# Performance work log

Hardware: AMD Instinct MI355X
Metric: run time of the kernel (lower is better)

The kernel has to match this reference:

```python
import jax, jax.numpy as jnp
import numpy as np

QMIN, QMAX = -128.0, 127.0          # int-8 symmetric range
CONST_N = 15.0                      # shift-exp range constant
OUT_BIT = 8                         # const_output_bit
INT32_MAX = 2.0 ** 31 - 1.0


def setup_inputs() -> dict:
    key = jax.random.key(0)
    kx, ks = jax.random.split(key)
    x = jax.random.normal(kx, (4, 2048, 4096), dtype=jnp.float32)
    # per-channel quantizer scale ~ abs-max / 127 statistics
    scaler = jnp.max(jnp.abs(x), axis=(0, 1)) / 127.0 + 1e-6  # [D]
    return {"x": x, "scaler": scaler}


def _int_exp_shift(x_int, sf):
    # x_int ~ integer-valued float tensor; sf per-channel scaling factor [D]
    x_int = x_int + jnp.floor(x_int / 2.0) - jnp.floor(x_int / 16.0)  # *1.4375 ~ /ln2
    x0 = jnp.floor(-1.0 / sf)                     # [D], negative
    x_int = jnp.maximum(x_int, CONST_N * x0)
    q = jnp.floor(x_int / x0)
    r = x_int - x0 * q
    e = r / 2.0 - x0
    return jnp.maximum(jnp.floor(e * jnp.exp2(CONST_N - q)), 0.0)


def reference(x, scaler):
    # quantize input per-channel (int8 grid, kept in float)
    pre_x_int = jnp.clip(jnp.round(x / scaler), QMIN, QMAX)
    sf_sig = scaler * 1.702

    x_int_max = jnp.max(pre_x_int, axis=-1, keepdims=True)   # [B,S,1]
    x_int = pre_x_int - x_int_max

    exp_int = _int_exp_shift(x_int, sf_sig)                  # [B,S,D]
    exp_int_max = _int_exp_shift(-x_int_max, sf_sig)         # [B,S,D] (bcast)
    exp_sum = jnp.minimum(exp_int + exp_int_max, INT32_MAX)

    factor = jnp.floor(INT32_MAX / exp_sum)
    sigmoid_int = jnp.floor(exp_int * factor / 2.0 ** (31 - OUT_BIT + 1))

    sigmoid_scale = 1.0 / 2.0 ** (OUT_BIT - 1)    # 1/128
    y = pre_x_int * sigmoid_int * (scaler * sigmoid_scale)
    return y
```

## Files before the change

### kernel.cpp

```cpp
#include <hip/hip_runtime.h>


#define D 4096
#define BLK 512
#define CPT 8
#define RPB 8
#define NW (BLK / 64)
#define NSLOT 12
#define TENT (NSLOT * 256)
#define EPS 1e-4f
#define F2_31 2147483648.0f

typedef float f32x4 __attribute__((ext_vector_type(4)));

__device__ __forceinline__ float exp_fast(float xi, float nx0, float rx0) {
    const float q = floorf(fmaf(xi, rx0, EPS));
    const float r = fmaf(nx0, q, xi);
    const float e = fmaf(r, 0.5f, nx0);
    return floorf(ldexpf(e, 15 - (int)q));
}

__device__ __forceinline__ float exp_slow(float xi, float x0) {
    xi = fmaxf(xi, 15.0f * x0);
    const float q = floorf(xi / x0);
    const float r = fmaf(-x0, q, xi);
    const float e = fmaf(r, 0.5f, -x0);
    return fmaxf(floorf(e * ldexpf(1.0f, 15 - (int)q)), 0.0f);
}

__global__ __launch_bounds__(BLK) void quantgelu_kernel(
    const float* __restrict__ x, const float* __restrict__ scaler,
    float* __restrict__ out, int nrows)
{
    const int tid  = threadIdx.x;
    const int wid  = tid >> 6;
    const int lane = tid & 63;
    const int row0 = blockIdx.x * RPB;

    __shared__ __align__(16) float smax2[2][NW];
    __shared__ float eit[TENT];
    __shared__ float siga[TENT];
    __shared__ float sigb[TENT];

    const int c0 = tid * 4;
    const int c1 = BLK * 4 + tid * 4;

    long long base = (long long)row0 * D;
    float4 xv[4];
    if (row0 < nrows) {
        xv[0] = *reinterpret_cast<const float4*>(x + base + c0);
        xv[1] = *reinterpret_cast<const float4*>(x + base + c1);
    }
    if (row0 + 1 < nrows) {
        xv[2] = *reinterpret_cast<const float4*>(x + base + D + c0);
        xv[3] = *reinterpret_cast<const float4*>(x + base + D + c1);
    }

    float s_[CPT], rs_[CPT], x0_[CPT];
    #pragma unroll
    for (int k = 0; k < 2; ++k) {
        const float4 sv = *reinterpret_cast<const float4*>(scaler + (k ? c1 : c0));
        const float ss[4] = {sv.x, sv.y, sv.z, sv.w};
        #pragma unroll
        for (int j = 0; j < 4; ++j) {
            const int i = k * 4 + j;
            const float s = ss[j];
            s_[i]  = s;
            rs_[i] = 1.0f / s;
            x0_[i] = floorf(-1.0f / (s * 1.702f));
        }
    }

    float x0mn = x0_[0], x0mx = x0_[0];
    #pragma unroll
    for (int i = 1; i < CPT; ++i) {
        x0mn = fminf(x0mn, x0_[i]);
        x0mx = fmaxf(x0mx, x0_[i]);
    }
    #pragma unroll
    for (int off = 1; off < 64; off <<= 1) {
        x0mn = fminf(x0mn, __shfl_xor(x0mn, off));
        x0mx = fmaxf(x0mx, __shfl_xor(x0mx, off));
    }
    if (lane == 0) { smax2[0][wid] = x0mn; smax2[1][wid] = x0mx; }
    __syncthreads();
    #pragma unroll
    for (int w = 0; w < NW; ++w) {
        x0mn = fminf(x0mn, smax2[0][w]);
        x0mx = fmaxf(x0mx, smax2[1][w]);
    }
    __syncthreads();

    const int  nslots = (int)(x0mx - x0mn) + 1;
    const bool ok = (x0mn >= -64.0f) && (nslots <= NSLOT);
    const int  nent = nslots << 8;

    int bo_[CPT];
    #pragma unroll
    for (int i = 0; i < CPT; ++i)
        bo_[i] = ((int)(x0_[i] - x0mn)) << 8;

    const float x0l  = x0mn + (float)lane;
    const float nx0l = -x0l;
    const float rx0l = 1.0f / x0l;
    const float c15l = 15.0f * x0l;

    if (ok) {
        for (int e = tid; e < nent; e += BLK) {
            const int   slot = e >> 8;
            const float x0v  = x0mn + (float)slot;
            float xi = -(float)(e & 255);
            xi = xi + floorf(xi * 0.5f) - floorf(xi * 0.0625f);
            xi = fmaxf(xi, 15.0f * x0v);
            eit[e] = exp_fast(xi, -x0v, __shfl(rx0l, slot));
        }
    }

    for (int g = 0; g < RPB / 2; ++g) {
        const int ra = row0 + 2 * g;
        if (ra >= nrows) break;
        const bool bval = (ra + 1) < nrows;

        float pa[CPT], pb[CPT];
        float va = -INFINITY, vb = -INFINITY;
        #pragma unroll
        for (int k = 0; k < 2; ++k) {
            const float* xa = reinterpret_cast<const float*>(&xv[k]);
            const float* xb = reinterpret_cast<const float*>(&xv[2 + k]);
            #pragma unroll
            for (int j = 0; j < 4; ++j) {
                const int i = k * 4 + j;
                float q0 = xa[j] * rs_[i];
                float rr = fmaf(-s_[i], q0, xa[j]);
                float p  = __builtin_amdgcn_fmed3f(
                               rintf(fmaf(rr, rs_[i], q0)), -128.0f, 127.0f);
                pa[i] = p;
                va = fmaxf(va, p);

                q0 = xb[j] * rs_[i];
                rr = fmaf(-s_[i], q0, xb[j]);
                p  = __builtin_amdgcn_fmed3f(
                               rintf(fmaf(rr, rs_[i], q0)), -128.0f, 127.0f);
                pb[i] = p;
                vb = fmaxf(vb, p);
            }
        }

        {
            const long long nb = base + 2 * D;
            if (ra + 2 < nrows) {
                xv[0] = *reinterpret_cast<const float4*>(x + nb + c0);
                xv[1] = *reinterpret_cast<const float4*>(x + nb + c1);
            }
            if (ra + 3 < nrows) {
                xv[2] = *reinterpret_cast<const float4*>(x + nb + D + c0);
                xv[3] = *reinterpret_cast<const float4*>(x + nb + D + c1);
            }
        }

        #pragma unroll
        for (int off = 1; off < 64; off <<= 1) {
            va = fmaxf(va, __shfl_xor(va, off));
            vb = fmaxf(vb, __shfl_xor(vb, off));
        }
        if (lane == 0) { smax2[0][wid] = va; smax2[1][wid] = vb; }
        __syncthreads();
        {
            const float4 a0 = *reinterpret_cast<const float4*>(&smax2[0][0]);
            const float4 a1 = *reinterpret_cast<const float4*>(&smax2[0][4]);
            const float4 b0 = *reinterpret_cast<const float4*>(&smax2[1][0]);
            const float4 b1 = *reinterpret_cast<const float4*>(&smax2[1][4]);
            va = fmaxf(fmaxf(fmaxf(a0.x, a0.y), fmaxf(a0.z, a0.w)),
                       fmaxf(fmaxf(a1.x, a1.y), fmaxf(a1.z, a1.w)));
            vb = fmaxf(fmaxf(fmaxf(b0.x, b0.y), fmaxf(b0.z, b0.w)),
                       fmaxf(fmaxf(b1.x, b1.y), fmaxf(b1.z, b1.w)));
        }

        const float xma  = -va, xmb = -vb;
        const float xmta = xma + floorf(xma * 0.5f) - floorf(xma * 0.0625f);
        const float xmtb = xmb + floorf(xmb * 0.5f) - floorf(xmb * 0.0625f);

        if (ok) {
            const float em_al = exp_fast(fmaxf(xmta, c15l), nx0l, rx0l);
            const float em_bl = bval ? exp_fast(fmaxf(xmtb, c15l), nx0l, rx0l) : 0.0f;
            for (int e = tid; e < nent; e += BLK) {
                const int   slot = e >> 8;
                const float ei   = eit[e];
                const float ema  = __shfl(em_al, slot);
                const float emb  = __shfl(em_bl, slot);
                const float fa = floorf(F2_31 / fminf(ei + ema, F2_31));
                const float fb = floorf(F2_31 / fminf(ei + emb, F2_31));
                siga[e] = floorf((ei * fa) * 0x1p-24f) * 0.0078125f;
                sigb[e] = floorf((ei * fb) * 0x1p-24f) * 0.0078125f;
            }
        }
        __syncthreads();

        if (ok) {
            #pragma unroll
            for (int k = 0; k < 2; ++k) {
                f32x4 ov;
                #pragma unroll
                for (int j = 0; j < 4; ++j) {
                    const int i = k * 4 + j;
                    const int d = (int)(va - pa[i]);
                    ov[j] = (pa[i] * siga[bo_[i] + d]) * s_[i];
                }
                __builtin_nontemporal_store(
                    ov, reinterpret_cast<f32x4*>(out + base + (k ? c1 : c0)));
            }
            if (bval) {
                #pragma unroll
                for (int k = 0; k < 2; ++k) {
                    f32x4 ov;
                    #pragma unroll
                    for (int j = 0; j < 4; ++j) {
                        const int i = k * 4 + j;
                        const int d = (int)(vb - pb[i]);
                        ov[j] = (pb[i] * sigb[bo_[i] + d]) * s_[i];
                    }
                    __builtin_nontemporal_store(
                        ov, reinterpret_cast<f32x4*>(out + base + D + (k ? c1 : c0)));
                }
            }
        } else {
            #pragma unroll
            for (int k = 0; k < 2; ++k) {
                f32x4 ov, ow;
                #pragma unroll
                for (int j = 0; j < 4; ++j) {
                    const int i = k * 4 + j;
                    const float x0   = x0_[i];
                    const float s128 = s_[i] * 0.0078125f;
                    {
                        float xi = pa[i] - va;
                        xi = xi + floorf(xi * 0.5f) - floorf(xi * 0.0625f);
                        const float ei = exp_slow(xi, x0);
                        const float em = exp_slow(xmta, x0);
                        const float factor = floorf(F2_31 / fminf(ei + em, F2_31));
                        ov[j] = (pa[i] * floorf((ei * factor) * 0x1p-24f)) * s128;
                    }
                    {
                        float xi = pb[i] - vb;
                        xi = xi + floorf(xi * 0.5f) - floorf(xi * 0.0625f);
                        const float ei = exp_slow(xi, x0);
                        const float em = exp_slow(xmtb, x0);
                        const float factor = floorf(F2_31 / fminf(ei + em, F2_31));
                        ow[j] = (pb[i] * floorf((ei * factor) * 0x1p-24f)) * s128;
                    }
                }
                __builtin_nontemporal_store(
                    ov, reinterpret_cast<f32x4*>(out + base + (k ? c1 : c0)));
                if (bval)
                    __builtin_nontemporal_store(
                        ow, reinterpret_cast<f32x4*>(out + base + D + (k ? c1 : c0)));
            }
        }

        base += 2 * D;
    }
}

extern "C" void kernel_launch(void* const* d_in, const int* in_sizes, int n_in,
                              void* d_out, int out_size, void* d_ws, size_t ws_size,
                              hipStream_t stream) {
    const float* x      = (const float*)d_in[0];
    const float* scaler = (const float*)d_in[1];
    float* out          = (float*)d_out;

    const int nrows = in_sizes[0] / D;
    const int grid  = (nrows + RPB - 1) / RPB;
    quantgelu_kernel<<<grid, BLK, 0, stream>>>(x, scaler, out, nrows);
}
```

Baseline: 53.07 us.

## Software-pipeline rows one at a time with double-buffered sigmoid tables

Replaces the two-rows-per-iteration loop with a one-row loop that quantizes and reduces the next row's max while building the current row's sigmoid table. The sigmoid table and the max slots are double-buffered, so each row needs only one block barrier instead of two. This also cuts register pressure: two float4 loads are held instead of four, and x0 is no longer kept per channel (the slow path recomputes it). The cost is that each row now builds its own table serially, with half the prefetch depth and more loop iterations.

```diff
diff --git a/kernel.cpp b/kernel.cpp
--- a/kernel.cpp
+++ b/kernel.cpp
@@ -39,66 +39,64 @@
 
     __shared__ __align__(16) float smax2[2][NW];
     __shared__ float eit[TENT];
-    __shared__ float siga[TENT];
-    __shared__ float sigb[TENT];
+    __shared__ float sig2[2][TENT];
 
     const int c0 = tid * 4;
     const int c1 = BLK * 4 + tid * 4;
 
-    long long base = (long long)row0 * D;
-    float4 xv[4];
+    float4 xv[2];
     if (row0 < nrows) {
-        xv[0] = *reinterpret_cast<const float4*>(x + base + c0);
-        xv[1] = *reinterpret_cast<const float4*>(x + base + c1);
-    }
-    if (row0 + 1 < nrows) {
-        xv[2] = *reinterpret_cast<const float4*>(x + base + D + c0);
-        xv[3] = *reinterpret_cast<const float4*>(x + base + D + c1);
-    }
-
-    float s_[CPT], rs_[CPT], x0_[CPT];
-    #pragma unroll
-    for (int k = 0; k < 2; ++k) {
-        const float4 sv = *reinterpret_cast<const float4*>(scaler + (k ? c1 : c0));
-        const float ss[4] = {sv.x, sv.y, sv.z, sv.w};
-        #pragma unroll
-        for (int j = 0; j < 4; ++j) {
-            const int i = k * 4 + j;
-            const float s = ss[j];
-            s_[i]  = s;
-            rs_[i] = 1.0f / s;
-            x0_[i] = floorf(-1.0f / (s * 1.702f));
-        }
-    }
-
-    float x0mn = x0_[0], x0mx = x0_[0];
-    #pragma unroll
-    for (int i = 1; i < CPT; ++i) {
-        x0mn = fminf(x0mn, x0_[i]);
-        x0mx = fmaxf(x0mx, x0_[i]);
-    }
-    #pragma unroll
-    for (int off = 1; off < 64; off <<= 1) {
-        x0mn = fminf(x0mn, __shfl_xor(x0mn, off));
-        x0mx = fmaxf(x0mx, __shfl_xor(x0mx, off));
-    }
-    if (lane == 0) { smax2[0][wid] = x0mn; smax2[1][wid] = x0mx; }
-    __syncthreads();
-    #pragma unroll
-    for (int w = 0; w < NW; ++w) {
-        x0mn = fminf(x0mn, smax2[0][w]);
-        x0mx = fmaxf(x0mx, smax2[1][w]);
-    }
-    __syncthreads();
+        const long long b0 = (long long)row0 * D;
+        xv[0] = *reinterpret_cast<const float4*>(x + b0 + c0);
+        xv[1] = *reinterpret_cast<const float4*>(x + b0 + c1);
+    }
+
+    float s_[CPT], rs_[CPT];
+    int   bo_[CPT];
+    float x0mn, x0mx;
+    {
+        float x0t[CPT];
+        #pragma unroll
+        for (int k = 0; k < 2; ++k) {
+            const float4 sv = *reinterpret_cast<const float4*>(scaler + (k ? c1 : c0));
+            const float ss[4] = {sv.x, sv.y, sv.z, sv.w};
+            #pragma unroll
+            for (int j = 0; j < 4; ++j) {
+                const int i = k * 4 + j;
+                const float s = ss[j];
+                s_[i]  = s;
+                rs_[i] = 1.0f / s;
+                x0t[i] = floorf(-1.0f / (s * 1.702f));
+            }
+        }
+        x0mn = x0t[0]; x0mx = x0t[0];
+        #pragma unroll
+        for (int i = 1; i < CPT; ++i) {
+            x0mn = fminf(x0mn, x0t[i]);
+            x0mx = fmaxf(x0mx, x0t[i]);
+        }
+        #pragma unroll
+        for (int off = 1; off < 64; off <<= 1) {
+            x0mn = fminf(x0mn, __shfl_xor(x0mn, off));
+            x0mx = fmaxf(x0mx, __shfl_xor(x0mx, off));
+        }
+        if (lane == 0) { smax2[0][wid] = x0mn; smax2[1][wid] = x0mx; }
+        __syncthreads();
+        #pragma unroll
+        for (int w = 0; w < NW; ++w) {
+            x0mn = fminf(x0mn, smax2[0][w]);
+            x0mx = fmaxf(x0mx, smax2[1][w]);
+        }
+        __syncthreads();
+
+        #pragma unroll
+        for (int i = 0; i < CPT; ++i)
+            bo_[i] = ((int)(x0t[i] - x0mn)) << 8;
+    }
 
     const int  nslots = (int)(x0mx - x0mn) + 1;
     const bool ok = (x0mn >= -64.0f) && (nslots <= NSLOT);
     const int  nent = nslots << 8;
-
-    int bo_[CPT];
-    #pragma unroll
-    for (int i = 0; i < CPT; ++i)
-        bo_[i] = ((int)(x0_[i] - x0mn)) << 8;
 
     const float x0l  = x0mn + (float)lane;
     const float nx0l = -x0l;
@@ -116,86 +114,91 @@
         }
     }
 
-    for (int g = 0; g < RPB / 2; ++g) {
-        const int ra = row0 + 2 * g;
-        if (ra >= nrows) break;
-        const bool bval = (ra + 1) < nrows;
-
-        float pa[CPT], pb[CPT];
-        float va = -INFINITY, vb = -INFINITY;
+    float pre_c[CPT], pre_n[CPT];
+    float vmax = -INFINITY;
+    if (row0 < nrows) {
         #pragma unroll
         for (int k = 0; k < 2; ++k) {
             const float* xa = reinterpret_cast<const float*>(&xv[k]);
-            const float* xb = reinterpret_cast<const float*>(&xv[2 + k]);
             #pragma unroll
             for (int j = 0; j < 4; ++j) {
                 const int i = k * 4 + j;
-                float q0 = xa[j] * rs_[i];
-                float rr = fmaf(-s_[i], q0, xa[j]);
-                float p  = __builtin_amdgcn_fmed3f(
-                               rintf(fmaf(rr, rs_[i], q0)), -128.0f, 127.0f);
-                pa[i] = p;
-                va = fmaxf(va, p);
-
-                q0 = xb[j] * rs_[i];
-                rr = fmaf(-s_[i], q0, xb[j]);
-                p  = __builtin_amdgcn_fmed3f(
-                               rintf(fmaf(rr, rs_[i], q0)), -128.0f, 127.0f);
-                pb[i] = p;
-                vb = fmaxf(vb, p);
-            }
-        }
-
-        {
-            const long long nb = base + 2 * D;
-            if (ra + 2 < nrows) {
-                xv[0] = *reinterpret_cast<const float4*>(x + nb + c0);
-                xv[1] = *reinterpret_cast<const float4*>(x + nb + c1);
-            }
-            if (ra + 3 < nrows) {
-                xv[2] = *reinterpret_cast<const float4*>(x + nb + D + c0);
-                xv[3] = *reinterpret_cast<const float4*>(x + nb + D + c1);
-            }
-        }
-
-        #pragma unroll
-        for (int off = 1; off < 64; off <<= 1) {
-            va = fmaxf(va, __shfl_xor(va, off));
-            vb = fmaxf(vb, __shfl_xor(vb, off));
-        }
-        if (lane == 0) { smax2[0][wid] = va; smax2[1][wid] = vb; }
-        __syncthreads();
-        {
-            const float4 a0 = *reinterpret_cast<const float4*>(&smax2[0][0]);
-            const float4 a1 = *reinterpret_cast<const float4*>(&smax2[0][4]);
-            const float4 b0 = *reinterpret_cast<const float4*>(&smax2[1][0]);
-            const float4 b1 = *reinterpret_cast<const float4*>(&smax2[1][4]);
-            va = fmaxf(fmaxf(fmaxf(a0.x, a0.y), fmaxf(a0.z, a0.w)),
-                       fmaxf(fmaxf(a1.x, a1.y), fmaxf(a1.z, a1.w)));
-            vb = fmaxf(fmaxf(fmaxf(b0.x, b0.y), fmaxf(b0.z, b0.w)),
-                       fmaxf(fmaxf(b1.x, b1.y), fmaxf(b1.z, b1.w)));
-        }
-
-        const float xma  = -va, xmb = -vb;
-        const float xmta = xma + floorf(xma * 0.5f) - floorf(xma * 0.0625f);
-        const float xmtb = xmb + floorf(xmb * 0.5f) - floorf(xmb * 0.0625f);
+                const float q0 = xa[j] * rs_[i];
+                const float rr = fmaf(-s_[i], q0, xa[j]);
+                const float p  = __builtin_amdgcn_fmed3f(
+                                   rintf(fmaf(rr, rs_[i], q0)), -128.0f, 127.0f);
+                pre_c[i] = p;
+                vmax = fmaxf(vmax, p);
+            }
+        }
+        #pragma unroll
+        for (int off = 1; off < 64; off <<= 1)
+            vmax = fmaxf(vmax, __shfl_xor(vmax, off));
+        if (lane == 0) smax2[0][wid] = vmax;
+        if (row0 + 1 < nrows) {
+            const long long b1 = (long long)(row0 + 1) * D;
+            xv[0] = *reinterpret_cast<const float4*>(x + b1 + c0);
+            xv[1] = *reinterpret_cast<const float4*>(x + b1 + c1);
+        }
+    }
+    __syncthreads();
+    {
+        const float4 a0 = *reinterpret_cast<const float4*>(&smax2[0][0]);
+        const float4 a1 = *reinterpret_cast<const float4*>(&smax2[0][4]);
+        vmax = fmaxf(fmaxf(fmaxf(a0.x, a0.y), fmaxf(a0.z, a0.w)),
+                     fmaxf(fmaxf(a1.x, a1.y), fmaxf(a1.z, a1.w)));
+    }
+
+    for (int r = 0; r < RPB; ++r) {
+        const int row = row0 + r;
+        if (row >= nrows) break;
+        const bool hasnext = (r + 1 < RPB) && (row + 1 < nrows);
+        const int  cur = r & 1, nxt = cur ^ 1;
+
+        const float xm  = -vmax;
+        const float xmt = xm + floorf(xm * 0.5f) - floorf(xm * 0.0625f);
 
         if (ok) {
-            const float em_al = exp_fast(fmaxf(xmta, c15l), nx0l, rx0l);
-            const float em_bl = bval ? exp_fast(fmaxf(xmtb, c15l), nx0l, rx0l) : 0.0f;
+            const float em_l = exp_fast(fmaxf(xmt, c15l), nx0l, rx0l);
             for (int e = tid; e < nent; e += BLK) {
                 const int   slot = e >> 8;
                 const float ei   = eit[e];
-                const float ema  = __shfl(em_al, slot);
-                const float emb  = __shfl(em_bl, slot);
-                const float fa = floorf(F2_31 / fminf(ei + ema, F2_31));
-                const float fb = floorf(F2_31 / fminf(ei + emb, F2_31));
-                siga[e] = floorf((ei * fa) * 0x1p-24f) * 0.0078125f;
-                sigb[e] = floorf((ei * fb) * 0x1p-24f) * 0.0078125f;
-            }
-        }
+                const float em   = __shfl(em_l, slot);
+                const float f    = floorf(F2_31 / fminf(ei + em, F2_31));
+                sig2[cur][e] = floorf((ei * f) * 0x1p-24f) * 0.0078125f;
+            }
+        }
+
+        if (hasnext) {
+            float vnext = -INFINITY;
+            #pragma unroll
+            for (int k = 0; k < 2; ++k) {
+                const float* xa = reinterpret_cast<const float*>(&xv[k]);
+                #pragma unroll
+                for (int j = 0; j < 4; ++j) {
+                    const int i = k * 4 + j;
+                    const float q0 = xa[j] * rs_[i];
+                    const float rr = fmaf(-s_[i], q0, xa[j]);
+                    const float p  = __builtin_amdgcn_fmed3f(
+                                       rintf(fmaf(rr, rs_[i], q0)), -128.0f, 127.0f);
+                    pre_n[i] = p;
+                    vnext = fmaxf(vnext, p);
+                }
+            }
+            #pragma unroll
+            for (int off = 1; off < 64; off <<= 1)
+                vnext = fmaxf(vnext, __shfl_xor(vnext, off));
+            if (lane == 0) smax2[nxt][wid] = vnext;
+            if (r + 2 < RPB && row + 2 < nrows) {
+                const long long b2 = (long long)(row + 2) * D;
+                xv[0] = *reinterpret_cast<const float4*>(x + b2 + c0);
+                xv[1] = *reinterpret_cast<const float4*>(x + b2 + c1);
+            }
+        }
+
         __syncthreads();
 
+        const long long rb = (long long)row * D;
         if (ok) {
             #pragma unroll
             for (int k = 0; k < 2; ++k) {
@@ -203,61 +206,41 @@
                 #pragma unroll
                 for (int j = 0; j < 4; ++j) {
                     const int i = k * 4 + j;
-                    const int d = (int)(va - pa[i]);
-                    ov[j] = (pa[i] * siga[bo_[i] + d]) * s_[i];
+                    const int d = (int)(vmax - pre_c[i]);
+                    ov[j] = (pre_c[i] * sig2[cur][bo_[i] + d]) * s_[i];
                 }
                 __builtin_nontemporal_store(
-                    ov, reinterpret_cast<f32x4*>(out + base + (k ? c1 : c0)));
-            }
-            if (bval) {
-                #pragma unroll
-                for (int k = 0; k < 2; ++k) {
-                    f32x4 ov;
-                    #pragma unroll
-                    for (int j = 0; j < 4; ++j) {
-                        const int i = k * 4 + j;
-                        const int d = (int)(vb - pb[i]);
-                        ov[j] = (pb[i] * sigb[bo_[i] + d]) * s_[i];
-                    }
-                    __builtin_nontemporal_store(
-                        ov, reinterpret_cast<f32x4*>(out + base + D + (k ? c1 : c0)));
-                }
+                    ov, reinterpret_cast<f32x4*>(out + rb + (k ? c1 : c0)));
             }
         } else {
             #pragma unroll
             for (int k = 0; k < 2; ++k) {
-                f32x4 ov, ow;
+                f32x4 ov;
                 #pragma unroll
                 for (int j = 0; j < 4; ++j) {
                     const int i = k * 4 + j;
-                    const float x0   = x0_[i];
-                    const float s128 = s_[i] * 0.0078125f;
-                    {
-                        float xi = pa[i] - va;
-                        xi = xi + floorf(xi * 0.5f) - floorf(xi * 0.0625f);
-                        const float ei = exp_slow(xi, x0);
-                        const float em = exp_slow(xmta, x0);
-                        const float factor = floorf(F2_31 / fminf(ei + em, F2_31));
-                        ov[j] = (pa[i] * floorf((ei * factor) * 0x1p-24f)) * s128;
-                    }
-                    {
-                        float xi = pb[i] - vb;
-                        xi = xi + floorf(xi * 0.5f) - floorf(xi * 0.0625f);
-                        const float ei = exp_slow(xi, x0);
-                        const float em = exp_slow(xmtb, x0);
-                        const float factor = floorf(F2_31 / fminf(ei + em, F2_31));
-                        ow[j] = (pb[i] * floorf((ei * factor) * 0x1p-24f)) * s128;
-                    }
+                    const float x0 = floorf(-1.0f / (s_[i] * 1.702f));
+                    float xi = pre_c[i] - vmax;
+                    xi = xi + floorf(xi * 0.5f) - floorf(xi * 0.0625f);
+                    const float ei = exp_slow(xi, x0);
+                    const float em = exp_slow(xmt, x0);
+                    const float factor = floorf(F2_31 / fminf(ei + em, F2_31));
+                    ov[j] = (pre_c[i] * floorf((ei * factor) * 0x1p-24f))
+                            * (s_[i] * 0.0078125f);
                 }
                 __builtin_nontemporal_store(
-                    ov, reinterpret_cast<f32x4*>(out + base + (k ? c1 : c0)));
-                if (bval)
-                    __builtin_nontemporal_store(
-                        ow, reinterpret_cast<f32x4*>(out + base + D + (k ? c1 : c0)));
-            }
-        }
-
-        base += 2 * D;
+                    ov, reinterpret_cast<f32x4*>(out + rb + (k ? c1 : c0)));
+            }
+        }
+
+        if (hasnext) {
+            const float4 a0 = *reinterpret_cast<const float4*>(&smax2[nxt][0]);
+            const float4 a1 = *reinterpret_cast<const float4*>(&smax2[nxt][4]);
+            vmax = fmaxf(fmaxf(fmaxf(a0.x, a0.y), fmaxf(a0.z, a0.w)),
+                         fmaxf(fmaxf(a1.x, a1.y), fmaxf(a1.z, a1.w)));
+            #pragma unroll
+            for (int i = 0; i < CPT; ++i) pre_c[i] = pre_n[i];
+        }
     }
 }
 
```

After: 49.37 us. -7.0%, faster.
